# Kernel optimization log

Hardware: AMD Instinct MI355X
Metric: run time of the kernel (lower is better)

Reference implementation:

```python
import jax, jax.numpy as jnp
import numpy as np

EPS = 1e-7  # K.epsilon()

def setup_inputs() -> dict:
    key = jax.random.key(0)
    ks = jax.random.split(key, 7)
    B, T, D, P, H = 64, 2048, 1024, 512, 2
    scale = 0.05  # keras 'uniform' init is small; keep activations in tanh range
    x = jax.random.normal(ks[0], (B, T, D), dtype=jnp.float32)
    proj_head = jax.random.normal(ks[1], (D, P), dtype=jnp.float32) * scale
    proj_prep = jax.random.normal(ks[2], (D, P), dtype=jnp.float32) * scale
    proj_child = jax.random.normal(ks[3], (D, P), dtype=jnp.float32) * scale
    hidden_W = jax.random.normal(ks[4], (H, P, P), dtype=jnp.float32) * scale
    scorer = jax.random.normal(ks[5], (P, 1), dtype=jnp.float32) * scale
    mask = jax.random.randint(ks[6], (B, T), 0, 2) > 0
    return {"x": x, "proj_head": proj_head, "proj_prep": proj_prep,
            "proj_child": proj_child, "hidden_W": hidden_W,
            "scorer": scorer, "mask": mask}

def reference(x, proj_head, proj_prep, proj_child, hidden_W, scorer, mask):
    # x: [B, T, D]; last two timesteps are preposition and child.
    head_enc = x[:, :-2, :]                       # [B, T-2, D]
    prep_enc = x[:, -2, :]                        # [B, D]
    child_enc = x[:, -1, :]                       # [B, D]
    head_proj = jnp.einsum('btd,dp->btp', head_enc, proj_head)      # [B, T-2, P]
    prep_proj = (prep_enc @ proj_prep)[:, None, :]                   # [B, 1, P]
    child_proj = (child_enc @ proj_child)[:, None, :]                # [B, 1, P]
    # composition_type == 'HPCT'
    composed = jnp.tanh(head_proj + prep_proj + child_proj)          # [B, T-2, P]
    for i in range(hidden_W.shape[0]):
        composed = jnp.tanh(jnp.einsum('btp,pq->btq', composed, hidden_W[i]))
    scores = jnp.einsum('btp,ps->bts', composed, scorer)[..., 0]     # [B, T-2]
    # masked softmax (custom: exp / masked-sum, not renormalized log-softmax)
    exp_scores = jnp.exp(scores)
    head_mask = mask[:, :-2]
    masked_exp = jnp.where(head_mask, exp_scores, 0.0)
    exp_sum = jnp.sum(masked_exp, axis=1, keepdims=True) + EPS
    return masked_exp / exp_sum
```

## Files before the change

kernel.cpp:

```cpp
#include <hip/hip_runtime.h>

typedef unsigned short u16;
typedef float f32x4 __attribute__((ext_vector_type(4)));
typedef unsigned int uint4v __attribute__((ext_vector_type(4)));

#define TT 2048
#define THEAD 2046
#define DD 1024
#define PP 512

#define LGKM0 asm volatile("s_waitcnt lgkmcnt(0)" ::: "memory")
#define VMC(n) asm volatile("s_waitcnt vmcnt(" #n ")" ::: "memory")
#define SB0 __builtin_amdgcn_sched_barrier(0)
#define BAR __builtin_amdgcn_s_barrier()

__device__ __forceinline__ u16 f2bf(float f) {
  unsigned int u = __float_as_uint(f);
  return (u16)((u + 0x7fffu + ((u >> 16) & 1u)) >> 16);
}
__device__ __forceinline__ float bf2f(u16 h) {
  return __uint_as_float(((unsigned int)h) << 16);
}
__device__ __forceinline__ float tanh_fast(float x) {
  float cx = fminf(fmaxf(x, -15.f), 15.f);
  float e = __expf(2.f * cx);
  return (e - 1.f) * __builtin_amdgcn_rcpf(e + 1.f);
}
__device__ __forceinline__ void cp16(const void* g, void* l) {
  __builtin_amdgcn_global_load_lds(
      (const __attribute__((address_space(1))) unsigned int*)g,
      (__attribute__((address_space(3))) unsigned int*)l, 16, 0, 0);
}
__device__ __forceinline__ void mfma16(f32x4& c, uint4v a, uint4v b) {
  asm("v_mfma_f32_16x16x32_bf16 %0, %1, %2, %0" : "+v"(c) : "v"(a), "v"(b));
}
__device__ __forceinline__ int ct_idx(int r, int p) {
  return (r << 9) + (p ^ ((r & 7) << 3));
}
__device__ __forceinline__ void stageW(const u16* __restrict__ src, int K,
                                       u16* dst, int k0, int lane) {
  const int rlo = lane >> 3;
  const int scol = (((lane & 7) ^ rlo) << 3) + k0;
#pragma unroll
  for (int i = 0; i < 8; ++i)
    cp16(src + (size_t)((i << 3) + rlo) * K + scol, dst + (i << 9));
}
__device__ __forceinline__ void at_write(u16* At, float4 v0, float4 v1,
                                         int r_st, int kp) {
  uint4 pk;
  pk.x = (unsigned)f2bf(v0.x) | ((unsigned)f2bf(v0.y) << 16);
  pk.y = (unsigned)f2bf(v0.z) | ((unsigned)f2bf(v0.w) << 16);
  pk.z = (unsigned)f2bf(v1.x) | ((unsigned)f2bf(v1.y) << 16);
  pk.w = (unsigned)f2bf(v1.z) | ((unsigned)f2bf(v1.w) << 16);
  *(uint4*)((char*)At + (r_st << 7) + ((kp ^ (r_st & 7)) << 4)) = pk;
}

__global__ __launch_bounds__(256) void cvt_k(const float* __restrict__ ph,
                                             const float* __restrict__ hw,
                                             u16* __restrict__ phT,
                                             u16* __restrict__ w0T,
                                             u16* __restrict__ w1T) {
  __shared__ float tl[32][33];
  const int bid = blockIdx.x, tid = threadIdx.x;
  const float* src;
  u16* dst;
  int SC, SR, r0, c0;
  if (bid < 512) {
    int tr = bid >> 4, tc = bid & 15;
    src = ph; SC = 512; dst = phT; SR = 1024; r0 = tr * 32; c0 = tc * 32;
  } else if (bid < 768) {
    int i = bid - 512; int tr = i >> 4, tc = i & 15;
    src = hw; SC = 512; dst = w0T; SR = 512; r0 = tr * 32; c0 = tc * 32;
  } else {
    int i = bid - 768; int tr = i >> 4, tc = i & 15;
    src = hw + 512 * 512; SC = 512; dst = w1T; SR = 512; r0 = tr * 32; c0 = tc * 32;
  }
  for (int i = tid; i < 1024; i += 256) {
    int r = i >> 5, c = i & 31;
    tl[r][c] = src[(size_t)(r0 + r) * SC + c0 + c];
  }
  __syncthreads();
  for (int i = tid; i < 1024; i += 256) {
    int r = i >> 5, c = i & 31;
    dst[(size_t)(c0 + r) * SR + r0 + c] = f2bf(tl[c][r]);
  }
}

__global__ __launch_bounds__(256) void bias_k(const float* __restrict__ x,
                                              const float* __restrict__ pp,
                                              const float* __restrict__ pc,
                                              float* __restrict__ bias) {
  const int b = blockIdx.x >> 3, pt = blockIdx.x & 7, tid = threadIdx.x;
  __shared__ float sprep[DD], schild[DD];
  __shared__ float red[4][64];
  for (int i = tid; i < DD; i += 256) {
    sprep[i] = x[((size_t)b * TT + (TT - 2)) * DD + i];
    schild[i] = x[((size_t)b * TT + (TT - 1)) * DD + i];
  }
  __syncthreads();
  const int pl = tid & 63, kq = tid >> 6;
  const int p = pt * 64 + pl;
  float s = 0.f;
  for (int k = kq * 256; k < kq * 256 + 256; ++k)
    s += sprep[k] * pp[(size_t)k * PP + p] + schild[k] * pc[(size_t)k * PP + p];
  red[kq][pl] = s;
  __syncthreads();
  if (tid < 64)
    bias[(size_t)b * PP + pt * 64 + tid] =
        red[0][tid] + red[1][tid] + red[2][tid] + red[3][tid];
}

__global__ __launch_bounds__(512) void fused_main(
    const float* __restrict__ x, const u16* __restrict__ phT,
    const u16* __restrict__ w0T, const u16* __restrict__ w1T,
    const float* __restrict__ bias, const float* __restrict__ scorer,
    const int* __restrict__ mask, float* __restrict__ out,
    float* __restrict__ partials) {
  __shared__ u16 Bt[PP * 64];
  __shared__ u16 AtL[2][64 * 64];
  __shared__ u16 Ct[64 * 512];
  __shared__ float ssc[PP];
  __shared__ float sred[64];

  const int tile = blockIdx.x, b = blockIdx.y;
  const int tid = threadIdx.x;
  const int lane = tid & 63, wid = tid >> 6;
  const int lr = lane & 15, kg = lane >> 4;

  const u16* phTw = phT + ((size_t)(wid << 6)) * DD;
  const u16* w0Tw = w0T + ((size_t)(wid << 6)) * PP;
  const u16* w1Tw = w1T + ((size_t)(wid << 6)) * PP;
  u16* BtW = Bt + (wid << 12);

  f32x4 acc[4][4];
#pragma unroll
  for (int mr = 0; mr < 4; ++mr)
#pragma unroll
    for (int nr = 0; nr < 4; ++nr) acc[mr][nr] = (f32x4){0.f, 0.f, 0.f, 0.f};

  const int r_st = tid >> 3, kp = tid & 7;
  const float* xptr = x + ((size_t)b * TT + tile * 64 + r_st) * DD + (kp << 3);

  ssc[tid] = scorer[tid];
  float bv[4];
#pragma unroll
  for (int nr = 0; nr < 4; ++nr)
    bv[nr] = bias[(b << 9) + (wid << 6) + (nr << 4) + lr];
  float4 x00 = *(const float4*)(xptr);
  float4 x01 = *(const float4*)(xptr + 4);
  VMC(0);
  at_write(AtL[0], x00, x01, r_st, kp);
  stageW(phTw, DD, BtW, 0, lane);
  SB0;
  float4 xa0 = *(const float4*)(xptr + 64);
  float4 xa1 = *(const float4*)(xptr + 68);
  float4 xb0, xb1;
  LGKM0;

#define ASTEP(K, XC0, XC1, XN0, XN1)                                           \
  {                                                                            \
    if ((K) < 15) { VMC(2); } else { VMC(0); }                                 \
    BAR;                                                                       \
    uint4v bfr0[4], bfr1[4], af0[4], af1[4];                                   \
    _Pragma("unroll") for (int nr = 0; nr < 4; ++nr) {                         \
      const int nl = (nr << 4) + lr;                                           \
      const char* bp = (const char*)BtW + (nl << 7);                           \
      bfr0[nr] = *(const uint4v*)(bp + ((kg << 4) ^ ((nl & 7) << 4)));         \
      bfr1[nr] = *(const uint4v*)(bp + ((64 + (kg << 4)) ^ ((nl & 7) << 4)));  \
    }                                                                          \
    _Pragma("unroll") for (int mr = 0; mr < 4; ++mr) {                         \
      const int r = (mr << 4) + lr;                                            \
      const char* ap = (const char*)AtL[(K) & 1] + (r << 7);                   \
      af0[mr] = *(const uint4v*)(ap + ((kg << 4) ^ ((r & 7) << 4)));           \
      af1[mr] = *(const uint4v*)(ap + ((64 + (kg << 4)) ^ ((r & 7) << 4)));    \
    }                                                                          \
    LGKM0;                                                                     \
    if ((K) < 15) stageW(phTw, DD, BtW, ((K) + 1) << 6, lane);                 \
    else          stageW(w0Tw, PP, BtW, 0, lane);                              \
    if ((K) < 15) at_write(AtL[((K) & 1) ^ 1], XC0, XC1, r_st, kp);            \
    SB0;                                                                       \
    if ((K) < 14) {                                                            \
      XN0 = *(const float4*)(xptr + (((K) + 2) << 6));                         \
      XN1 = *(const float4*)(xptr + (((K) + 2) << 6) + 4);                     \
    }                                                                          \
    __builtin_amdgcn_s_setprio(1);                                             \
    _Pragma("unroll") for (int mr = 0; mr < 4; ++mr)                           \
      _Pragma("unroll") for (int nr = 0; nr < 4; ++nr)                         \
        mfma16(acc[mr][nr], af0[mr], bfr0[nr]);                                \
    _Pragma("unroll") for (int mr = 0; mr < 4; ++mr)                           \
      _Pragma("unroll") for (int nr = 0; nr < 4; ++nr)                         \
        mfma16(acc[mr][nr], af1[mr], bfr1[nr]);                                \
    __builtin_amdgcn_s_setprio(0);                                             \
    LGKM0;                                                                     \
  }

#pragma unroll
  for (int kk = 0; kk < 8; ++kk) {
    ASTEP(2 * kk, xa0, xa1, xb0, xb1);
    ASTEP(2 * kk + 1, xb0, xb1, xa0, xa1);
  }

#pragma unroll
  for (int mr = 0; mr < 4; ++mr)
#pragma unroll
    for (int nr = 0; nr < 4; ++nr) {
      const int c = (wid << 6) + (nr << 4) + lr;
      const int r0 = (mr << 4) + (kg << 2);
#pragma unroll
      for (int j = 0; j < 4; ++j)
        Ct[ct_idx(r0 + j, c)] = f2bf(tanh_fast(acc[mr][nr][j] + bv[nr]));
    }
  LGKM0;
  BAR;

#define BSTEP(K, CURW, NXTW, DONEXT)                                           \
  {                                                                            \
    VMC(0);                                                                    \
    uint4v bfr0[4], bfr1[4], af0[4], af1[4];                                   \
    _Pragma("unroll") for (int nr = 0; nr < 4; ++nr) {                         \
      const int nl = (nr << 4) + lr;                                           \
      const char* bp = (const char*)BtW + (nl << 7);                           \
      bfr0[nr] = *(const uint4v*)(bp + ((kg << 4) ^ ((nl & 7) << 4)));         \
      bfr1[nr] = *(const uint4v*)(bp + ((64 + (kg << 4)) ^ ((nl & 7) << 4)));  \
    }                                                                          \
    _Pragma("unroll") for (int mr = 0; mr < 4; ++mr) {                         \
      const int r = (mr << 4) + lr;                                            \
      af0[mr] = *(const uint4v*)&Ct[ct_idx(r, ((K) << 6) + (kg << 3))];        \
      af1[mr] = *(const uint4v*)&Ct[ct_idx(r, ((K) << 6) + 32 + (kg << 3))];   \
    }                                                                          \
    LGKM0;                                                                     \
    if ((K) < 7)       stageW(CURW, PP, BtW, ((K) + 1) << 6, lane);            \
    else if (DONEXT)   stageW(NXTW, PP, BtW, 0, lane);                         \
    __builtin_amdgcn_s_setprio(1);                                             \
    _Pragma("unroll") for (int mr = 0; mr < 4; ++mr)                           \
      _Pragma("unroll") for (int nr = 0; nr < 4; ++nr)                         \
        mfma16(acc[mr][nr], af0[mr], bfr0[nr]);                                \
    _Pragma("unroll") for (int mr = 0; mr < 4; ++mr)                           \
      _Pragma("unroll") for (int nr = 0; nr < 4; ++nr)                         \
        mfma16(acc[mr][nr], af1[mr], bfr1[nr]);                                \
    __builtin_amdgcn_s_setprio(0);                                             \
  }

#pragma unroll
  for (int mr = 0; mr < 4; ++mr)
#pragma unroll
    for (int nr = 0; nr < 4; ++nr) acc[mr][nr] = (f32x4){0.f, 0.f, 0.f, 0.f};
#pragma unroll
  for (int k = 0; k < 8; ++k) BSTEP(k, w0Tw, w1Tw, true);
  BAR;
#pragma unroll
  for (int mr = 0; mr < 4; ++mr)
#pragma unroll
    for (int nr = 0; nr < 4; ++nr) {
      const int c = (wid << 6) + (nr << 4) + lr;
      const int r0 = (mr << 4) + (kg << 2);
#pragma unroll
      for (int j = 0; j < 4; ++j)
        Ct[ct_idx(r0 + j, c)] = f2bf(tanh_fast(acc[mr][nr][j]));
    }
  LGKM0;
  BAR;

#pragma unroll
  for (int mr = 0; mr < 4; ++mr)
#pragma unroll
    for (int nr = 0; nr < 4; ++nr) acc[mr][nr] = (f32x4){0.f, 0.f, 0.f, 0.f};
#pragma unroll
  for (int k = 0; k < 8; ++k) BSTEP(k, w1Tw, w1Tw, false);
  BAR;
#pragma unroll
  for (int mr = 0; mr < 4; ++mr)
#pragma unroll
    for (int nr = 0; nr < 4; ++nr) {
      const int c = (wid << 6) + (nr << 4) + lr;
      const int r0 = (mr << 4) + (kg << 2);
#pragma unroll
      for (int j = 0; j < 4; ++j)
        Ct[ct_idx(r0 + j, c)] = f2bf(tanh_fast(acc[mr][nr][j]));
    }
  __syncthreads();

  {
    const int r = tid >> 3, j = tid & 7;
    const int p0 = j << 6;
    float s = 0.f;
#pragma unroll
    for (int i = 0; i < 8; ++i) {
      uint4v v = *(const uint4v*)&Ct[ct_idx(r, p0 + (i << 3))];
      const float* sc = &ssc[p0 + (i << 3)];
#pragma unroll
      for (int e = 0; e < 4; ++e) {
        unsigned int u = v[e];
        s += bf2f((u16)(u & 0xffffu)) * sc[e * 2] +
             bf2f((u16)(u >> 16)) * sc[e * 2 + 1];
      }
    }
    s += __shfl_down(s, 4, 8);
    s += __shfl_down(s, 2, 8);
    s += __shfl_down(s, 1, 8);
    if (j == 0) {
      const int tg = (tile << 6) + r;
      float e = 0.f;
      if (tg < THEAD && mask[(size_t)b * TT + tg] != 0) e = __expf(s);
      if (tg < THEAD) out[(size_t)b * THEAD + tg] = e;
      sred[r] = e;
    }
    __syncthreads();
    if (tid < 64) {
      float v = sred[tid];
      v += __shfl_down(v, 32);
      v += __shfl_down(v, 16);
      v += __shfl_down(v, 8);
      v += __shfl_down(v, 4);
      v += __shfl_down(v, 2);
      v += __shfl_down(v, 1);
      if (tid == 0) partials[(b << 5) + tile] = v;
    }
  }
}

__global__ __launch_bounds__(256) void norm_k(float* __restrict__ out,
                                              const float* __restrict__ partials) {
  const int b = blockIdx.y, j = blockIdx.x, tid = threadIdx.x;
  __shared__ float sinv;
  if (tid < 32) {
    float v = partials[(b << 5) + tid];
    v += __shfl_down(v, 16, 32);
    v += __shfl_down(v, 8, 32);
    v += __shfl_down(v, 4, 32);
    v += __shfl_down(v, 2, 32);
    v += __shfl_down(v, 1, 32);
    if (tid == 0) sinv = 1.f / (v + 1e-7f);
  }
  __syncthreads();
  const int t = (j << 8) + tid;
  if (t < THEAD) out[(size_t)b * THEAD + t] *= sinv;
}

extern "C" void kernel_launch(void* const* d_in, const int* in_sizes, int n_in,
                              void* d_out, int out_size, void* d_ws, size_t ws_size,
                              hipStream_t stream) {
  const float* x  = (const float*)d_in[0];
  const float* ph = (const float*)d_in[1];
  const float* pp = (const float*)d_in[2];
  const float* pc = (const float*)d_in[3];
  const float* hw = (const float*)d_in[4];
  const float* sc = (const float*)d_in[5];
  const int* mask = (const int*)d_in[6];
  float* out = (float*)d_out;

  char* ws = (char*)d_ws;
  u16* phT = (u16*)ws;
  u16* w0T = (u16*)(ws + (1 << 20));
  u16* w1T = (u16*)(ws + (1 << 20) + (1 << 19));
  float* biasb = (float*)(ws + (1 << 21));
  float* partials = (float*)(ws + (1 << 21) + 131072);

  cvt_k<<<1024, 256, 0, stream>>>(ph, hw, phT, w0T, w1T);
  bias_k<<<512, 256, 0, stream>>>(x, pp, pc, biasb);
  fused_main<<<dim3(32, 64), 512, 0, stream>>>(x, phT, w0T, w1T, biasb, sc,
                                               mask, out, partials);
  norm_k<<<dim3(8, 64), 256, 0, stream>>>(out, partials);
}
```

Baseline: 437.6 us.

## Load weight fragments directly to registers and cut LDS to raise occupancy

Drops the LDS staging of weight tiles through global_load_lds. Each wave now loads its B fragments straight from global memory into registers, double-buffered across half-k steps, and the A tile becomes single-buffered. The Ct swizzle gains an extra XOR term, the scorer is read from global memory, and launch bounds request 4 blocks per CU. The aim is to free LDS and cut barrier and staging overhead so more blocks can be resident, at the cost of uncoalesced per-lane global weight reads and higher register pressure.

```diff
diff --git a/kernel.cpp b/kernel.cpp
--- a/kernel.cpp
+++ b/kernel.cpp
@@ -10,7 +10,6 @@
 #define PP 512
 
 #define LGKM0 asm volatile("s_waitcnt lgkmcnt(0)" ::: "memory")
-#define VMC(n) asm volatile("s_waitcnt vmcnt(" #n ")" ::: "memory")
 #define SB0 __builtin_amdgcn_sched_barrier(0)
 #define BAR __builtin_amdgcn_s_barrier()
 
@@ -26,34 +25,61 @@
   float e = __expf(2.f * cx);
   return (e - 1.f) * __builtin_amdgcn_rcpf(e + 1.f);
 }
-__device__ __forceinline__ void cp16(const void* g, void* l) {
-  __builtin_amdgcn_global_load_lds(
-      (const __attribute__((address_space(1))) unsigned int*)g,
-      (__attribute__((address_space(3))) unsigned int*)l, 16, 0, 0);
-}
 __device__ __forceinline__ void mfma16(f32x4& c, uint4v a, uint4v b) {
   asm("v_mfma_f32_16x16x32_bf16 %0, %1, %2, %0" : "+v"(c) : "v"(a), "v"(b));
 }
 __device__ __forceinline__ int ct_idx(int r, int p) {
-  return (r << 9) + (p ^ ((r & 7) << 3));
-}
-__device__ __forceinline__ void stageW(const u16* __restrict__ src, int K,
-                                       u16* dst, int k0, int lane) {
-  const int rlo = lane >> 3;
-  const int scol = (((lane & 7) ^ rlo) << 3) + k0;
-#pragma unroll
-  for (int i = 0; i < 8; ++i)
-    cp16(src + (size_t)((i << 3) + rlo) * K + scol, dst + (i << 9));
-}
-__device__ __forceinline__ void at_write(u16* At, float4 v0, float4 v1,
-                                         int r_st, int kp) {
+  return (r << 9) + (p ^ (((r & 7) ^ ((p >> 6) & 7)) << 3));
+}
+__device__ __forceinline__ uint4 cvt4(float4 v0, float4 v1) {
   uint4 pk;
   pk.x = (unsigned)f2bf(v0.x) | ((unsigned)f2bf(v0.y) << 16);
   pk.y = (unsigned)f2bf(v0.z) | ((unsigned)f2bf(v0.w) << 16);
   pk.z = (unsigned)f2bf(v1.x) | ((unsigned)f2bf(v1.y) << 16);
   pk.w = (unsigned)f2bf(v1.z) | ((unsigned)f2bf(v1.w) << 16);
-  *(uint4*)((char*)At + (r_st << 7) + ((kp ^ (r_st & 7)) << 4)) = pk;
-}
+  return pk;
+}
+
+#define AT_CLUSTER(HALF, BF)                                                   \
+  {                                                                            \
+    const int co_ = (((((HALF) << 2) + kg) ^ (lr & 7)) << 4);                  \
+    uint4v a0_, a1_;                                                           \
+    a0_ = *(const uint4v*)((const char*)At + ((0 + lr) << 7) + co_);           \
+    a1_ = *(const uint4v*)((const char*)At + ((16 + lr) << 7) + co_);          \
+    __builtin_amdgcn_s_setprio(1);                                             \
+    mfma16(acc[0][0], a0_, BF[0]); mfma16(acc[0][1], a0_, BF[1]);              \
+    mfma16(acc[0][2], a0_, BF[2]); mfma16(acc[0][3], a0_, BF[3]);              \
+    mfma16(acc[1][0], a1_, BF[0]); mfma16(acc[1][1], a1_, BF[1]);              \
+    mfma16(acc[1][2], a1_, BF[2]); mfma16(acc[1][3], a1_, BF[3]);              \
+    a0_ = *(const uint4v*)((const char*)At + ((32 + lr) << 7) + co_);          \
+    a1_ = *(const uint4v*)((const char*)At + ((48 + lr) << 7) + co_);          \
+    mfma16(acc[2][0], a0_, BF[0]); mfma16(acc[2][1], a0_, BF[1]);              \
+    mfma16(acc[2][2], a0_, BF[2]); mfma16(acc[2][3], a0_, BF[3]);              \
+    mfma16(acc[3][0], a1_, BF[0]); mfma16(acc[3][1], a1_, BF[1]);              \
+    mfma16(acc[3][2], a1_, BF[2]); mfma16(acc[3][3], a1_, BF[3]);              \
+    __builtin_amdgcn_s_setprio(0);                                             \
+  }
+
+#define CT_CLUSTER(K, BF)                                                      \
+  {                                                                            \
+    const int p_ = ((K) << 5) + (kg << 3);                                     \
+    const int e_ = p_ ^ (((lr & 7) ^ ((p_ >> 6) & 7)) << 3);                   \
+    uint4v a0_, a1_;                                                           \
+    a0_ = *(const uint4v*)&Ct[((0 + lr) << 9) + e_];                           \
+    a1_ = *(const uint4v*)&Ct[((16 + lr) << 9) + e_];                          \
+    __builtin_amdgcn_s_setprio(1);                                             \
+    mfma16(acc[0][0], a0_, BF[0]); mfma16(acc[0][1], a0_, BF[1]);              \
+    mfma16(acc[0][2], a0_, BF[2]); mfma16(acc[0][3], a0_, BF[3]);              \
+    mfma16(acc[1][0], a1_, BF[0]); mfma16(acc[1][1], a1_, BF[1]);              \
+    mfma16(acc[1][2], a1_, BF[2]); mfma16(acc[1][3], a1_, BF[3]);              \
+    a0_ = *(const uint4v*)&Ct[((32 + lr) << 9) + e_];                          \
+    a1_ = *(const uint4v*)&Ct[((48 + lr) << 9) + e_];                          \
+    mfma16(acc[2][0], a0_, BF[0]); mfma16(acc[2][1], a0_, BF[1]);              \
+    mfma16(acc[2][2], a0_, BF[2]); mfma16(acc[2][3], a0_, BF[3]);              \
+    mfma16(acc[3][0], a1_, BF[0]); mfma16(acc[3][1], a1_, BF[1]);              \
+    mfma16(acc[3][2], a1_, BF[2]); mfma16(acc[3][3], a1_, BF[3]);              \
+    __builtin_amdgcn_s_setprio(0);                                             \
+  }
 
 __global__ __launch_bounds__(256) void cvt_k(const float* __restrict__ ph,
                                              const float* __restrict__ hw,
@@ -110,190 +136,159 @@
         red[0][tid] + red[1][tid] + red[2][tid] + red[3][tid];
 }
 
-__global__ __launch_bounds__(512) void fused_main(
+__global__ __launch_bounds__(512, 4) void fused_main(
     const float* __restrict__ x, const u16* __restrict__ phT,
     const u16* __restrict__ w0T, const u16* __restrict__ w1T,
     const float* __restrict__ bias, const float* __restrict__ scorer,
     const int* __restrict__ mask, float* __restrict__ out,
     float* __restrict__ partials) {
-  __shared__ u16 Bt[PP * 64];
-  __shared__ u16 AtL[2][64 * 64];
-  __shared__ u16 Ct[64 * 512];
-  __shared__ float ssc[PP];
-  __shared__ float sred[64];
+  __shared__ __align__(16) u16 At[64 * 64];
+  __shared__ __align__(16) u16 Ct[64 * 512];
 
   const int tile = blockIdx.x, b = blockIdx.y;
   const int tid = threadIdx.x;
   const int lane = tid & 63, wid = tid >> 6;
   const int lr = lane & 15, kg = lane >> 4;
-
-  const u16* phTw = phT + ((size_t)(wid << 6)) * DD;
-  const u16* w0Tw = w0T + ((size_t)(wid << 6)) * PP;
-  const u16* w1Tw = w1T + ((size_t)(wid << 6)) * PP;
-  u16* BtW = Bt + (wid << 12);
-
-  f32x4 acc[4][4];
-#pragma unroll
-  for (int mr = 0; mr < 4; ++mr)
-#pragma unroll
-    for (int nr = 0; nr < 4; ++nr) acc[mr][nr] = (f32x4){0.f, 0.f, 0.f, 0.f};
-
   const int r_st = tid >> 3, kp = tid & 7;
-  const float* xptr = x + ((size_t)b * TT + tile * 64 + r_st) * DD + (kp << 3);
-
-  ssc[tid] = scorer[tid];
+
+  const u16* __restrict__ phTw = phT + ((size_t)(wid << 6)) * DD;
+  const u16* __restrict__ w0Tw = w0T + ((size_t)(wid << 6)) * PP;
+  const u16* __restrict__ w1Tw = w1T + ((size_t)(wid << 6)) * PP;
+
+  int boffA[4], boffH[4];
+#pragma unroll
+  for (int nr = 0; nr < 4; ++nr) {
+    boffA[nr] = (((nr << 4) + lr) << 10) + (kg << 3);
+    boffH[nr] = (((nr << 4) + lr) << 9) + (kg << 3);
+  }
+
+  const float* __restrict__ xbase =
+      x + ((size_t)b * TT + tile * 64 + r_st) * DD + (kp << 3);
+  u16* atdst = (u16*)((char*)At + (r_st << 7) + ((kp ^ (r_st & 7)) << 4));
+
   float bv[4];
 #pragma unroll
   for (int nr = 0; nr < 4; ++nr)
     bv[nr] = bias[(b << 9) + (wid << 6) + (nr << 4) + lr];
-  float4 x00 = *(const float4*)(xptr);
-  float4 x01 = *(const float4*)(xptr + 4);
-  VMC(0);
-  at_write(AtL[0], x00, x01, r_st, kp);
-  stageW(phTw, DD, BtW, 0, lane);
-  SB0;
-  float4 xa0 = *(const float4*)(xptr + 64);
-  float4 xa1 = *(const float4*)(xptr + 68);
-  float4 xb0, xb1;
+
+  f32x4 acc[4][4];
+#pragma unroll
+  for (int mr = 0; mr < 4; ++mr)
+#pragma unroll
+    for (int nr = 0; nr < 4; ++nr) acc[mr][nr] = (f32x4){0.f, 0.f, 0.f, 0.f};
+
+  uint4v bC[4], bN[4];
+#pragma unroll
+  for (int nr = 0; nr < 4; ++nr) bC[nr] = *(const uint4v*)(phTw + boffA[nr]);
+  {
+    float4 v0 = *(const float4*)(xbase);
+    float4 v1 = *(const float4*)(xbase + 4);
+    uint4 pk = cvt4(v0, v1);
+    *(uint4*)atdst = pk;
+  }
   LGKM0;
-
-#define ASTEP(K, XC0, XC1, XN0, XN1)                                           \
-  {                                                                            \
-    if ((K) < 15) { VMC(2); } else { VMC(0); }                                 \
-    BAR;                                                                       \
-    uint4v bfr0[4], bfr1[4], af0[4], af1[4];                                   \
-    _Pragma("unroll") for (int nr = 0; nr < 4; ++nr) {                         \
-      const int nl = (nr << 4) + lr;                                           \
-      const char* bp = (const char*)BtW + (nl << 7);                           \
-      bfr0[nr] = *(const uint4v*)(bp + ((kg << 4) ^ ((nl & 7) << 4)));         \
-      bfr1[nr] = *(const uint4v*)(bp + ((64 + (kg << 4)) ^ ((nl & 7) << 4)));  \
-    }                                                                          \
-    _Pragma("unroll") for (int mr = 0; mr < 4; ++mr) {                         \
-      const int r = (mr << 4) + lr;                                            \
-      const char* ap = (const char*)AtL[(K) & 1] + (r << 7);                   \
-      af0[mr] = *(const uint4v*)(ap + ((kg << 4) ^ ((r & 7) << 4)));           \
-      af1[mr] = *(const uint4v*)(ap + ((64 + (kg << 4)) ^ ((r & 7) << 4)));    \
-    }                                                                          \
-    LGKM0;                                                                     \
-    if ((K) < 15) stageW(phTw, DD, BtW, ((K) + 1) << 6, lane);                 \
-    else          stageW(w0Tw, PP, BtW, 0, lane);                              \
-    if ((K) < 15) at_write(AtL[((K) & 1) ^ 1], XC0, XC1, r_st, kp);            \
-    SB0;                                                                       \
-    if ((K) < 14) {                                                            \
-      XN0 = *(const float4*)(xptr + (((K) + 2) << 6));                         \
-      XN1 = *(const float4*)(xptr + (((K) + 2) << 6) + 4);                     \
-    }                                                                          \
-    __builtin_amdgcn_s_setprio(1);                                             \
-    _Pragma("unroll") for (int mr = 0; mr < 4; ++mr)                           \
-      _Pragma("unroll") for (int nr = 0; nr < 4; ++nr)                         \
-        mfma16(acc[mr][nr], af0[mr], bfr0[nr]);                                \
-    _Pragma("unroll") for (int mr = 0; mr < 4; ++mr)                           \
-      _Pragma("unroll") for (int nr = 0; nr < 4; ++nr)                         \
-        mfma16(acc[mr][nr], af1[mr], bfr1[nr]);                                \
-    __builtin_amdgcn_s_setprio(0);                                             \
-    LGKM0;                                                                     \
-  }
-
-#pragma unroll
-  for (int kk = 0; kk < 8; ++kk) {
-    ASTEP(2 * kk, xa0, xa1, xb0, xb1);
-    ASTEP(2 * kk + 1, xb0, xb1, xa0, xa1);
-  }
+  BAR; SB0;
+
+#pragma unroll 1
+  for (int p = 0; p < 15; ++p) {
+    const u16* bkE = phTw + (p << 6);
+#pragma unroll
+    for (int nr = 0; nr < 4; ++nr)
+      bN[nr] = *(const uint4v*)(bkE + 32 + boffA[nr]);
+    float4 xv0 = *(const float4*)(xbase + ((p + 1) << 6));
+    float4 xv1 = *(const float4*)(xbase + ((p + 1) << 6) + 4);
+    AT_CLUSTER(0, bC);
+#pragma unroll
+    for (int nr = 0; nr < 4; ++nr)
+      bC[nr] = *(const uint4v*)(bkE + 64 + boffA[nr]);
+    uint4 pk = cvt4(xv0, xv1);
+    AT_CLUSTER(1, bN);
+    BAR;
+    *(uint4*)atdst = pk;
+    LGKM0;
+    BAR; SB0;
+  }
+#pragma unroll
+  for (int nr = 0; nr < 4; ++nr)
+    bN[nr] = *(const uint4v*)(phTw + 992 + boffA[nr]);
+  AT_CLUSTER(0, bC);
+#pragma unroll
+  for (int nr = 0; nr < 4; ++nr)
+    bC[nr] = *(const uint4v*)(w0Tw + boffH[nr]);
+  AT_CLUSTER(1, bN);
 
 #pragma unroll
   for (int mr = 0; mr < 4; ++mr)
 #pragma unroll
     for (int nr = 0; nr < 4; ++nr) {
       const int c = (wid << 6) + (nr << 4) + lr;
-      const int r0 = (mr << 4) + (kg << 2);
-#pragma unroll
-      for (int j = 0; j < 4; ++j)
-        Ct[ct_idx(r0 + j, c)] = f2bf(tanh_fast(acc[mr][nr][j] + bv[nr]));
+#pragma unroll
+      for (int j = 0; j < 4; ++j) {
+        const int r = (mr << 4) + (kg << 2) + j;
+        Ct[ct_idx(r, c)] = f2bf(tanh_fast(acc[mr][nr][j] + bv[nr]));
+      }
+      acc[mr][nr] = (f32x4){0.f, 0.f, 0.f, 0.f};
     }
   LGKM0;
-  BAR;
-
-#define BSTEP(K, CURW, NXTW, DONEXT)                                           \
-  {                                                                            \
-    VMC(0);                                                                    \
-    uint4v bfr0[4], bfr1[4], af0[4], af1[4];                                   \
-    _Pragma("unroll") for (int nr = 0; nr < 4; ++nr) {                         \
-      const int nl = (nr << 4) + lr;                                           \
-      const char* bp = (const char*)BtW + (nl << 7);                           \
-      bfr0[nr] = *(const uint4v*)(bp + ((kg << 4) ^ ((nl & 7) << 4)));         \
-      bfr1[nr] = *(const uint4v*)(bp + ((64 + (kg << 4)) ^ ((nl & 7) << 4)));  \
-    }                                                                          \
-    _Pragma("unroll") for (int mr = 0; mr < 4; ++mr) {                         \
-      const int r = (mr << 4) + lr;                                            \
-      af0[mr] = *(const uint4v*)&Ct[ct_idx(r, ((K) << 6) + (kg << 3))];        \
-      af1[mr] = *(const uint4v*)&Ct[ct_idx(r, ((K) << 6) + 32 + (kg << 3))];   \
-    }                                                                          \
-    LGKM0;                                                                     \
-    if ((K) < 7)       stageW(CURW, PP, BtW, ((K) + 1) << 6, lane);            \
-    else if (DONEXT)   stageW(NXTW, PP, BtW, 0, lane);                         \
-    __builtin_amdgcn_s_setprio(1);                                             \
-    _Pragma("unroll") for (int mr = 0; mr < 4; ++mr)                           \
-      _Pragma("unroll") for (int nr = 0; nr < 4; ++nr)                         \
-        mfma16(acc[mr][nr], af0[mr], bfr0[nr]);                                \
-    _Pragma("unroll") for (int mr = 0; mr < 4; ++mr)                           \
-      _Pragma("unroll") for (int nr = 0; nr < 4; ++nr)                         \
-        mfma16(acc[mr][nr], af1[mr], bfr1[nr]);                                \
-    __builtin_amdgcn_s_setprio(0);                                             \
-  }
-
-#pragma unroll
-  for (int mr = 0; mr < 4; ++mr)
-#pragma unroll
-    for (int nr = 0; nr < 4; ++nr) acc[mr][nr] = (f32x4){0.f, 0.f, 0.f, 0.f};
-#pragma unroll
-  for (int k = 0; k < 8; ++k) BSTEP(k, w0Tw, w1Tw, true);
-  BAR;
-#pragma unroll
-  for (int mr = 0; mr < 4; ++mr)
-#pragma unroll
-    for (int nr = 0; nr < 4; ++nr) {
-      const int c = (wid << 6) + (nr << 4) + lr;
-      const int r0 = (mr << 4) + (kg << 2);
-#pragma unroll
-      for (int j = 0; j < 4; ++j)
-        Ct[ct_idx(r0 + j, c)] = f2bf(tanh_fast(acc[mr][nr][j]));
-    }
-  LGKM0;
-  BAR;
-
-#pragma unroll
-  for (int mr = 0; mr < 4; ++mr)
-#pragma unroll
-    for (int nr = 0; nr < 4; ++nr) acc[mr][nr] = (f32x4){0.f, 0.f, 0.f, 0.f};
-#pragma unroll
-  for (int k = 0; k < 8; ++k) BSTEP(k, w1Tw, w1Tw, false);
-  BAR;
-#pragma unroll
-  for (int mr = 0; mr < 4; ++mr)
-#pragma unroll
-    for (int nr = 0; nr < 4; ++nr) {
-      const int c = (wid << 6) + (nr << 4) + lr;
-      const int r0 = (mr << 4) + (kg << 2);
-#pragma unroll
-      for (int j = 0; j < 4; ++j)
-        Ct[ct_idx(r0 + j, c)] = f2bf(tanh_fast(acc[mr][nr][j]));
-    }
-  __syncthreads();
+  BAR; SB0;
+
+#pragma unroll 1
+  for (int L = 0; L < 2; ++L) {
+    const u16* __restrict__ wT = L ? w1Tw : w0Tw;
+#pragma unroll 1
+    for (int kk = 0; kk < 8; ++kk) {
+      const int k = kk << 1;
+#pragma unroll
+      for (int nr = 0; nr < 4; ++nr)
+        bN[nr] = *(const uint4v*)(wT + ((k + 1) << 5) + boffH[nr]);
+      CT_CLUSTER(k, bC);
+      if (kk < 7) {
+#pragma unroll
+        for (int nr = 0; nr < 4; ++nr)
+          bC[nr] = *(const uint4v*)(wT + ((k + 2) << 5) + boffH[nr]);
+      } else if (L == 0) {
+#pragma unroll
+        for (int nr = 0; nr < 4; ++nr)
+          bC[nr] = *(const uint4v*)(w1Tw + boffH[nr]);
+      }
+      CT_CLUSTER(k + 1, bN);
+    }
+    BAR;
+#pragma unroll
+    for (int mr = 0; mr < 4; ++mr)
+#pragma unroll
+      for (int nr = 0; nr < 4; ++nr) {
+        const int c = (wid << 6) + (nr << 4) + lr;
+#pragma unroll
+        for (int j = 0; j < 4; ++j) {
+          const int r = (mr << 4) + (kg << 2) + j;
+          Ct[ct_idx(r, c)] = f2bf(tanh_fast(acc[mr][nr][j]));
+        }
+        acc[mr][nr] = (f32x4){0.f, 0.f, 0.f, 0.f};
+      }
+    LGKM0;
+    BAR; SB0;
+  }
 
   {
+    float* sredp = (float*)At;
     const int r = tid >> 3, j = tid & 7;
     const int p0 = j << 6;
     float s = 0.f;
 #pragma unroll
     for (int i = 0; i < 8; ++i) {
       uint4v v = *(const uint4v*)&Ct[ct_idx(r, p0 + (i << 3))];
-      const float* sc = &ssc[p0 + (i << 3)];
-#pragma unroll
-      for (int e = 0; e < 4; ++e) {
-        unsigned int u = v[e];
-        s += bf2f((u16)(u & 0xffffu)) * sc[e * 2] +
-             bf2f((u16)(u >> 16)) * sc[e * 2 + 1];
-      }
+      float4 sc0 = *(const float4*)(scorer + p0 + (i << 3));
+      float4 sc1 = *(const float4*)(scorer + p0 + (i << 3) + 4);
+      unsigned int u;
+      u = v[0];
+      s += bf2f((u16)(u & 0xffffu)) * sc0.x + bf2f((u16)(u >> 16)) * sc0.y;
+      u = v[1];
+      s += bf2f((u16)(u & 0xffffu)) * sc0.z + bf2f((u16)(u >> 16)) * sc0.w;
+      u = v[2];
+      s += bf2f((u16)(u & 0xffffu)) * sc1.x + bf2f((u16)(u >> 16)) * sc1.y;
+      u = v[3];
+      s += bf2f((u16)(u & 0xffffu)) * sc1.z + bf2f((u16)(u >> 16)) * sc1.w;
     }
     s += __shfl_down(s, 4, 8);
     s += __shfl_down(s, 2, 8);
@@ -303,11 +298,11 @@
       float e = 0.f;
       if (tg < THEAD && mask[(size_t)b * TT + tg] != 0) e = __expf(s);
       if (tg < THEAD) out[(size_t)b * THEAD + tg] = e;
-      sred[r] = e;
+      sredp[r] = e;
     }
     __syncthreads();
     if (tid < 64) {
-      float v = sred[tid];
+      float v = sredp[tid];
       v += __shfl_down(v, 32);
       v += __shfl_down(v, 16);
       v += __shfl_down(v, 8);
```

After: 808.9 us. 1.85x slower.
